# Kernel tuning notes

Measured on AMD Instinct MI355X. Metric: run time of the kernel, lower is better.

The kernel has to match this reference:

```python
import jax, jax.numpy as jnp
import numpy as np

N_WIRES = 4
N_OPS = 20  # depth * 10
DIM = 2 ** N_WIRES

_CNOT4 = jnp.array([[1, 0, 0, 0],
                    [0, 1, 0, 0],
                    [0, 0, 0, 1],
                    [0, 0, 1, 0]], dtype=jnp.complex64)


def _ry(t):
    c, s = jnp.cos(t / 2), jnp.sin(t / 2)
    return jnp.stack([jnp.stack([c, -s], -1), jnp.stack([s, c], -1)], -2).astype(jnp.complex64)


def _rx(t):
    c = jnp.cos(t / 2).astype(jnp.complex64)
    s = (-1j) * jnp.sin(t / 2).astype(jnp.complex64)
    return jnp.stack([jnp.stack([c, s], -1), jnp.stack([s, c], -1)], -2)


def _rz(t):
    e = jnp.exp(-0.5j * t.astype(jnp.complex64))
    z = jnp.zeros_like(e)
    return jnp.stack([jnp.stack([e, z], -1), jnp.stack([z, jnp.conj(e)], -1)], -2)


def _apply_1q(state, U, w):
    # state: [B, 2^n]; U: [2,2] (shared) or [B,2,2] (per-batch angle)
    b = state.shape[0]
    left, right = 2 ** w, 2 ** (N_WIRES - w - 1)
    s = state.reshape(b, left, 2, right)
    if U.ndim == 2:
        s = jnp.einsum('ij,bajc->baic', U, s)
    else:
        s = jnp.einsum('bij,bajc->baic', U, s)
    return s.reshape(b, -1)


def _apply_cnot(state, c):
    # CNOT on adjacent wires (c, c+1)
    b = state.shape[0]
    left, right = 2 ** c, 2 ** (N_WIRES - c - 2)
    s = state.reshape(b, left, 4, right)
    s = jnp.einsum('ij,bajc->baic', _CNOT4, s)
    return s.reshape(b, -1)


def _circuit(x, y, theta):
    b = x.shape[0]
    state = jnp.zeros((b, DIM), jnp.complex64).at[:, 0].set(1.0)
    # encoder: Ry(x_w) on each wire
    for w in range(N_WIRES):
        state = _apply_1q(state, _ry(x[:, w]), w)
    # fixed pseudo-random layer of 20 gates (RX/RY/RZ rotations + CNOTs)
    rot = (_rx, _ry, _rz)
    for i in range(N_OPS):
        kind = i % 4
        if kind == 3:
            state = _apply_cnot(state, (i // 4) % (N_WIRES - 1))
        else:
            w = (7 * i + 3) % N_WIRES
            state = _apply_1q(state, rot[kind](theta[i]), w)
    # second encoder: Ry(-y_w)
    for w in range(N_WIRES):
        state = _apply_1q(state, _ry(-y[:, w]), w)
    # PauliZ expectation on wire 0, then abs (original: abs(measure(...)[0]))
    probs = state.real ** 2 + state.imag ** 2  # [B, 16]
    p = probs.reshape(b, 2, -1)
    z0 = jnp.sum(p[:, 0], -1) - jnp.sum(p[:, 1], -1)
    return jnp.abs(z0)


def setup_inputs() -> dict:
    key = jax.random.key(0)
    k1, k2, k3 = jax.random.split(key, 3)
    B = 262144
    x = jax.random.normal(k1, (B, N_WIRES), jnp.float32)
    y = jax.random.normal(k2, (B, N_WIRES), jnp.float32)
    theta = jax.random.normal(k3, (N_OPS,), jnp.float32)
    return {"x": x, "y": y, "theta": theta}


def reference(x, y, theta):
    return _circuit(x, y, theta)
```

## Files before the change

### kernel.cpp

```cpp
#include <hip/hip_runtime.h>
#include <hip/hip_bf16.h>
#include <math.h>


#define NWIRES 4

template<int W>
__device__ __forceinline__ void apply_ry(float (&sr)[16], float (&si)[16], float c, float s) {
    constexpr int bit = 1 << (3 - W);
    #pragma unroll
    for (int i = 0; i < 16; ++i) {
        if (!(i & bit)) {
            constexpr int dummy = 0; (void)dummy;
            const int j = i | bit;
            float ar = sr[i], ai = si[i], br = sr[j], bi = si[j];
            sr[i] = c * ar - s * br;
            si[i] = c * ai - s * bi;
            sr[j] = s * ar + c * br;
            si[j] = s * ai + c * bi;
        }
    }
}

template<int W>
__device__ __forceinline__ void apply_rx(float (&sr)[16], float (&si)[16], float c, float s) {
    constexpr int bit = 1 << (3 - W);
    #pragma unroll
    for (int i = 0; i < 16; ++i) {
        if (!(i & bit)) {
            const int j = i | bit;
            float ar = sr[i], ai = si[i], br = sr[j], bi = si[j];
            sr[i] = c * ar + s * bi;
            si[i] = c * ai - s * br;
            sr[j] = c * br + s * ai;
            si[j] = c * bi - s * ar;
        }
    }
}

template<int W>
__device__ __forceinline__ void apply_rz(float (&sr)[16], float (&si)[16], float c, float s) {
    constexpr int bit = 1 << (3 - W);
    #pragma unroll
    for (int i = 0; i < 16; ++i) {
        if (!(i & bit)) {
            const int j = i | bit;
            float ar = sr[i], ai = si[i], br = sr[j], bi = si[j];
            sr[i] = c * ar + s * ai;
            si[i] = c * ai - s * ar;
            sr[j] = c * br - s * bi;
            si[j] = c * bi + s * br;
        }
    }
}

template<int C>
__device__ __forceinline__ void apply_cnot(float (&sr)[16], float (&si)[16]) {
    constexpr int cb = 1 << (3 - C);
    constexpr int tb = 1 << (2 - C);
    #pragma unroll
    for (int i = 0; i < 16; ++i) {
        if ((i & cb) && !(i & tb)) {
            const int j = i | tb;
            float t;
            t = sr[i]; sr[i] = sr[j]; sr[j] = t;
            t = si[i]; si[i] = si[j]; si[j] = t;
        }
    }
}

__global__ __launch_bounds__(256) void qsim_kernel(
        const float* __restrict__ x,
        const float* __restrict__ y,
        const float* __restrict__ theta,
        float* __restrict__ out,
        int B) {
    int b = blockIdx.x * blockDim.x + threadIdx.x;
    if (b >= B) return;

    float4 xv = reinterpret_cast<const float4*>(x)[b];
    float y0  = y[4 * b];

    float c0, s0, c1, s1, c2, s2, c3, s3;
    __sincosf(0.5f * xv.x, &s0, &c0);
    __sincosf(0.5f * xv.y, &s1, &c1);
    __sincosf(0.5f * xv.z, &s2, &c2);
    __sincosf(0.5f * xv.w, &s3, &c3);

    float sr[16], si[16];
    #pragma unroll
    for (int i = 0; i < 16; ++i) {
        float p = ((i & 8) ? s0 : c0)
                * ((i & 4) ? s1 : c1)
                * ((i & 2) ? s2 : c2)
                * ((i & 1) ? s3 : c3);
        sr[i] = p;
        si[i] = 0.0f;
    }

    float tc, ts;
    #define ROT(IDX, FN, W) do { \
        __sincosf(0.5f * theta[IDX], &ts, &tc); \
        FN<W>(sr, si, tc, ts); \
    } while (0)

    ROT(0,  apply_rx, 3);
    ROT(1,  apply_ry, 2);
    ROT(2,  apply_rz, 1);
    apply_cnot<0>(sr, si);
    ROT(4,  apply_rx, 3);
    ROT(5,  apply_ry, 2);
    ROT(6,  apply_rz, 1);
    apply_cnot<1>(sr, si);
    ROT(8,  apply_rx, 3);
    ROT(9,  apply_ry, 2);
    ROT(10, apply_rz, 1);
    apply_cnot<2>(sr, si);
    ROT(12, apply_rx, 3);
    ROT(13, apply_ry, 2);
    ROT(14, apply_rz, 1);
    apply_cnot<0>(sr, si);
    ROT(16, apply_rx, 3);
    ROT(17, apply_ry, 2);
    ROT(18, apply_rz, 1);
    apply_cnot<1>(sr, si);
    #undef ROT

    float zacc = 0.0f, xacc = 0.0f;
    #pragma unroll
    for (int i = 0; i < 8; ++i) {
        float p0 = sr[i] * sr[i] + si[i] * si[i];
        float p1 = sr[i + 8] * sr[i + 8] + si[i + 8] * si[i + 8];
        zacc += p0 - p1;
        xacc += sr[i] * sr[i + 8] + si[i] * si[i + 8];
    }
    xacc *= 2.0f;

    float cy, sy;
    __sincosf(y0, &sy, &cy);
    out[b] = fabsf(cy * zacc + sy * xacc);
}

extern "C" void kernel_launch(void* const* d_in, const int* in_sizes, int n_in,
                              void* d_out, int out_size, void* d_ws, size_t ws_size,
                              hipStream_t stream) {
    const float* x     = (const float*)d_in[0];
    const float* y     = (const float*)d_in[1];
    const float* theta = (const float*)d_in[2];
    float* out = (float*)d_out;

    int B = out_size;
    int block = 256;
    int grid = (B + block - 1) / block;
    qsim_kernel<<<grid, block, 0, stream>>>(x, y, theta, out, B);
}
```

Before: 11.21 us.

## Precompute fixed-layer observable as quadratic form in prep kernel

Adds a single-block prep kernel that builds the 16x16 unitary of the theta-dependent gate layer and folds it with the Z and X observables into two symmetric 136-entry quadratic-form coefficient tables in workspace. The main kernel then evaluates two quadratic forms over the real product-state amplitudes instead of simulating 20 complex gates per sample. This removes most of the per-sample gate arithmetic but adds a second launch and 272 coefficient loads per thread, which should come from cache since every thread reads the same addresses.

```diff
diff --git a/kernel.cpp b/kernel.cpp
--- a/kernel.cpp
+++ b/kernel.cpp
@@ -2,8 +2,6 @@
 #include <hip/hip_bf16.h>
 #include <math.h>
 
-
-#define NWIRES 4
 
 template<int W>
 __device__ __forceinline__ void apply_ry(float (&sr)[16], float (&si)[16], float c, float s) {
@@ -11,13 +9,10 @@
     #pragma unroll
     for (int i = 0; i < 16; ++i) {
         if (!(i & bit)) {
-            constexpr int dummy = 0; (void)dummy;
             const int j = i | bit;
             float ar = sr[i], ai = si[i], br = sr[j], bi = si[j];
-            sr[i] = c * ar - s * br;
-            si[i] = c * ai - s * bi;
-            sr[j] = s * ar + c * br;
-            si[j] = s * ai + c * bi;
+            sr[i] = c * ar - s * br;  si[i] = c * ai - s * bi;
+            sr[j] = s * ar + c * br;  si[j] = s * ai + c * bi;
         }
     }
 }
@@ -30,10 +25,8 @@
         if (!(i & bit)) {
             const int j = i | bit;
             float ar = sr[i], ai = si[i], br = sr[j], bi = si[j];
-            sr[i] = c * ar + s * bi;
-            si[i] = c * ai - s * br;
-            sr[j] = c * br + s * ai;
-            si[j] = c * bi - s * ar;
+            sr[i] = c * ar + s * bi;  si[i] = c * ai - s * br;
+            sr[j] = c * br + s * ai;  si[j] = c * bi - s * ar;
         }
     }
 }
@@ -46,10 +39,8 @@
         if (!(i & bit)) {
             const int j = i | bit;
             float ar = sr[i], ai = si[i], br = sr[j], bi = si[j];
-            sr[i] = c * ar + s * ai;
-            si[i] = c * ai - s * ar;
-            sr[j] = c * br - s * bi;
-            si[j] = c * bi + s * br;
+            sr[i] = c * ar + s * ai;  si[i] = c * ai - s * ar;
+            sr[j] = c * br - s * bi;  si[j] = c * bi + s * br;
         }
     }
 }
@@ -69,17 +60,65 @@
     }
 }
 
-__global__ __launch_bounds__(256) void qsim_kernel(
+__global__ __launch_bounds__(256) void qprep_kernel(
+        const float* __restrict__ theta, float* __restrict__ ws) {
+    __shared__ float Ur[16][16], Ui[16][16];
+    int t = threadIdx.x;
+    if (t < 16) {
+        float sr[16], si[16];
+        #pragma unroll
+        for (int i = 0; i < 16; ++i) { sr[i] = (i == t) ? 1.0f : 0.0f; si[i] = 0.0f; }
+        float tc, ts;
+        #define ROT(IDX, FN, W) do { \
+            __sincosf(0.5f * theta[IDX], &ts, &tc); \
+            FN<W>(sr, si, tc, ts); \
+        } while (0)
+        ROT(0,  apply_rx, 3); ROT(1,  apply_ry, 2); ROT(2,  apply_rz, 1);
+        apply_cnot<0>(sr, si);
+        ROT(4,  apply_rx, 3); ROT(5,  apply_ry, 2); ROT(6,  apply_rz, 1);
+        apply_cnot<1>(sr, si);
+        ROT(8,  apply_rx, 3); ROT(9,  apply_ry, 2); ROT(10, apply_rz, 1);
+        apply_cnot<2>(sr, si);
+        ROT(12, apply_rx, 3); ROT(13, apply_ry, 2); ROT(14, apply_rz, 1);
+        apply_cnot<0>(sr, si);
+        ROT(16, apply_rx, 3); ROT(17, apply_ry, 2); ROT(18, apply_rz, 1);
+        apply_cnot<1>(sr, si);
+        #undef ROT
+        #pragma unroll
+        for (int k = 0; k < 16; ++k) { Ur[k][t] = sr[k]; Ui[k][t] = si[k]; }
+    }
+    __syncthreads();
+    if (t < 136) {
+        int p = t, i = 0, len = 16;
+        while (p >= len) { p -= len; --len; ++i; }
+        int j = i + p;
+        float sa = 0.0f, sb = 0.0f;
+        #pragma unroll
+        for (int k = 0; k < 16; ++k) {
+            float uri = Ur[k][i], uii = Ui[k][i];
+            float zr  = Ur[k][j], zi  = Ui[k][j];
+            float xr  = Ur[k ^ 8][j], xi = Ui[k ^ 8][j];
+            float sgn = (k < 8) ? 1.0f : -1.0f;
+            sa += sgn * (uri * zr + uii * zi);
+            sb += uri * xr + uii * xi;
+        }
+        float w = (i == j) ? 1.0f : 2.0f;
+        ws[t]       = w * sa;
+        ws[136 + t] = w * sb;
+    }
+}
+
+__global__ __launch_bounds__(256) void qmain_kernel(
         const float* __restrict__ x,
         const float* __restrict__ y,
-        const float* __restrict__ theta,
+        const float* __restrict__ ws,
         float* __restrict__ out,
         int B) {
     int b = blockIdx.x * blockDim.x + threadIdx.x;
     if (b >= B) return;
 
     float4 xv = reinterpret_cast<const float4*>(x)[b];
-    float y0  = y[4 * b];
+    float y0  = reinterpret_cast<const float4*>(y)[b].x;
 
     float c0, s0, c1, s1, c2, s2, c3, s3;
     __sincosf(0.5f * xv.x, &s0, &c0);
@@ -87,58 +126,30 @@
     __sincosf(0.5f * xv.z, &s2, &c2);
     __sincosf(0.5f * xv.w, &s3, &c3);
 
-    float sr[16], si[16];
+    float q0[4] = { c0 * c1, c0 * s1, s0 * c1, s0 * s1 };
+    float q1[4] = { c2 * c3, c2 * s3, s2 * c3, s2 * s3 };
+    float psi[16];
+    #pragma unroll
+    for (int i = 0; i < 16; ++i) psi[i] = q0[i >> 2] * q1[i & 3];
+
+    const float* A  = ws;
+    const float* Bm = ws + 136;
+    float a = 0.0f, bb = 0.0f;
+    int p = 0;
     #pragma unroll
     for (int i = 0; i < 16; ++i) {
-        float p = ((i & 8) ? s0 : c0)
-                * ((i & 4) ? s1 : c1)
-                * ((i & 2) ? s2 : c2)
-                * ((i & 1) ? s3 : c3);
-        sr[i] = p;
-        si[i] = 0.0f;
+        #pragma unroll
+        for (int j = i; j < 16; ++j) {
+            float t2 = psi[i] * psi[j];
+            a  = fmaf(A[p],  t2, a);
+            bb = fmaf(Bm[p], t2, bb);
+            ++p;
+        }
     }
-
-    float tc, ts;
-    #define ROT(IDX, FN, W) do { \
-        __sincosf(0.5f * theta[IDX], &ts, &tc); \
-        FN<W>(sr, si, tc, ts); \
-    } while (0)
-
-    ROT(0,  apply_rx, 3);
-    ROT(1,  apply_ry, 2);
-    ROT(2,  apply_rz, 1);
-    apply_cnot<0>(sr, si);
-    ROT(4,  apply_rx, 3);
-    ROT(5,  apply_ry, 2);
-    ROT(6,  apply_rz, 1);
-    apply_cnot<1>(sr, si);
-    ROT(8,  apply_rx, 3);
-    ROT(9,  apply_ry, 2);
-    ROT(10, apply_rz, 1);
-    apply_cnot<2>(sr, si);
-    ROT(12, apply_rx, 3);
-    ROT(13, apply_ry, 2);
-    ROT(14, apply_rz, 1);
-    apply_cnot<0>(sr, si);
-    ROT(16, apply_rx, 3);
-    ROT(17, apply_ry, 2);
-    ROT(18, apply_rz, 1);
-    apply_cnot<1>(sr, si);
-    #undef ROT
-
-    float zacc = 0.0f, xacc = 0.0f;
-    #pragma unroll
-    for (int i = 0; i < 8; ++i) {
-        float p0 = sr[i] * sr[i] + si[i] * si[i];
-        float p1 = sr[i + 8] * sr[i + 8] + si[i + 8] * si[i + 8];
-        zacc += p0 - p1;
-        xacc += sr[i] * sr[i + 8] + si[i] * si[i + 8];
-    }
-    xacc *= 2.0f;
 
     float cy, sy;
     __sincosf(y0, &sy, &cy);
-    out[b] = fabsf(cy * zacc + sy * xacc);
+    out[b] = fabsf(cy * a + sy * bb);
 }
 
 extern "C" void kernel_launch(void* const* d_in, const int* in_sizes, int n_in,
@@ -148,9 +159,11 @@
     const float* y     = (const float*)d_in[1];
     const float* theta = (const float*)d_in[2];
     float* out = (float*)d_out;
+    float* ws  = (float*)d_ws;
 
     int B = out_size;
+    qprep_kernel<<<1, 256, 0, stream>>>(theta, ws);
     int block = 256;
     int grid = (B + block - 1) / block;
-    qsim_kernel<<<grid, block, 0, stream>>>(x, y, theta, out, B);
+    qmain_kernel<<<grid, block, 0, stream>>>(x, y, ws, out, B);
 }
```

Result: slower. 15.50 us (+38.4%).
